# Kernel tuning notes

Hardware: AMD Instinct MI355X
Metric: run time of the kernel (lower is better)

## Reference

```python
import jax, jax.numpy as jnp
import numpy as np

T, N, ENC_DIM, DEC_DIM, ATTN_DIM = 2048, 64, 1024, 1024, 256


def setup_inputs() -> dict:
    key = jax.random.key(0)
    k1, k2, k3, k4, k5 = jax.random.split(key, 5)
    enc_out = jax.random.normal(k1, (T, N, ENC_DIM), dtype=jnp.float32)
    dec_h = jax.random.normal(k2, (N, DEC_DIM), dtype=jnp.float32)
    # Linear weights stored as [out, in] like torch; scaled like default init
    W_e = jax.random.normal(k3, (ATTN_DIM, ENC_DIM), dtype=jnp.float32) / np.sqrt(ENC_DIM)
    W_d = jax.random.normal(k4, (ATTN_DIM, DEC_DIM), dtype=jnp.float32) / np.sqrt(DEC_DIM)
    v = jax.random.normal(k5, (1, ATTN_DIM), dtype=jnp.float32) / np.sqrt(ATTN_DIM)
    return {"enc_out": enc_out, "dec_h": dec_h, "W_e": W_e, "W_d": W_d, "v": v}


def reference(enc_out, dec_h, W_e, W_d, v):
    # e_proj: [T, N, A]; d_proj: [1, N, A]
    e_proj = jnp.einsum('tne,ae->tna', enc_out, W_e)
    d_proj = jnp.einsum('nd,ad->na', dec_h, W_d)[None, :, :]
    # scores: [T, N] = tanh(e+d) @ v
    scores = jnp.einsum('tna,a->tn', jnp.tanh(e_proj + d_proj), v[0])
    alpha = jax.nn.softmax(scores, axis=0)  # softmax over time dim
    ctx = jnp.einsum('tn,tne->ne', alpha, enc_out)  # [N, E]
    return (ctx, alpha)
```

## Files before the change

kernel.cpp:

```cpp
#include <hip/hip_runtime.h>
#include <math.h>

#define T_DIM 2048
#define N_DIM 64
#define E_DIM 1024
#define A_DIM 256
#define TCHUNK 32
#define NCHUNK (T_DIM / TCHUNK)

typedef __bf16 bf16x8 __attribute__((ext_vector_type(8)));
typedef __bf16 bf16x4 __attribute__((ext_vector_type(4)));
typedef float f32x4 __attribute__((ext_vector_type(4)));

__device__ __forceinline__ float tanh_fast(float x) {
    float xc = fminf(fmaxf(x, -15.f), 15.f);
    float e = __expf(2.f * xc);
    return (e - 1.f) / (e + 1.f);
}

__device__ __forceinline__ void lds_barrier() {
    asm volatile("s_waitcnt lgkmcnt(0)\n\ts_barrier" ::: "memory");
}

__global__ __launch_bounds__(256) void prep_kernel(
    const float* __restrict__ W_e, const float* __restrict__ dec_h,
    const float* __restrict__ W_d, __bf16* __restrict__ Wp,
    float* __restrict__ d_proj) {
    __shared__ float dec[E_DIM];
    const int tid = threadIdx.x;
    if (blockIdx.x < 128) {
        const int uid = blockIdx.x * 256 + tid;
        const int a = uid >> 7;
        const int c = uid & 127;
        const float4* src = (const float4*)(W_e + (size_t)a * E_DIM + c * 8);
        float4 x0 = src[0], x1 = src[1];
        bf16x8 o;
        o[0] = (__bf16)x0.x; o[1] = (__bf16)x0.y; o[2] = (__bf16)x0.z; o[3] = (__bf16)x0.w;
        o[4] = (__bf16)x1.x; o[5] = (__bf16)x1.y; o[6] = (__bf16)x1.z; o[7] = (__bf16)x1.w;
        *(bf16x8*)(Wp + ((size_t)c * 256 + a) * 8) = o;
    } else {
        const int n = blockIdx.x - 128;
        reinterpret_cast<float4*>(dec)[tid] =
            reinterpret_cast<const float4*>(dec_h + (size_t)n * E_DIM)[tid];
        __syncthreads();
        const float* w = W_d + (size_t)tid * E_DIM;
        float acc = 0.f;
#pragma unroll 4
        for (int e = 0; e < E_DIM; e += 4) {
            float4 wv = *reinterpret_cast<const float4*>(w + e);
            acc = fmaf(wv.x, dec[e], acc);
            acc = fmaf(wv.y, dec[e + 1], acc);
            acc = fmaf(wv.z, dec[e + 2], acc);
            acc = fmaf(wv.w, dec[e + 3], acc);
        }
        d_proj[n * A_DIM + tid] = acc;
    }
}

__global__ __launch_bounds__(512, 4) void flash_kernel(
    const float* __restrict__ enc, const __bf16* __restrict__ Wp,
    const float* __restrict__ dproj, const float* __restrict__ v,
    float* __restrict__ scores, float* __restrict__ partial,
    float* __restrict__ ms, float* __restrict__ zs) {
    __shared__ __align__(16) __bf16 Atile[TCHUNK * E_DIM];
    float* red = ((float*)Atile) + 16384 - 288;
    float* wls = red + 256;

    const int tid = threadIdx.x;
    const int bid = blockIdx.x;
    const int n = bid & (N_DIM - 1);
    const int c = bid >> 6;
    const int t0 = c * TCHUNK;
    const int wn = tid >> 6;
    const int lane = tid & 63;
    const int lr = lane & 15, lg = lane >> 4;

    f32x4 acc[2][2];
#pragma unroll
    for (int i = 0; i < 2; ++i)
#pragma unroll
        for (int j = 0; j < 2; ++j) acc[i][j] = (f32x4){0.f, 0.f, 0.f, 0.f};

    float vv[2], dp[2];
#pragma unroll
    for (int fn = 0; fn < 2; ++fn) {
        const int a = wn * 32 + fn * 16 + lr;
        vv[fn] = v[a];
        dp[fn] = dproj[n * A_DIM + a];
    }

    const int srow = tid >> 4, sg = tid & 15;
    const int sgg = (sg & 7) >> 1, sbh = sg & 1;
    const int sks = sg >> 3;
    const float* encRow =
        enc + ((size_t)(t0 + srow) * N_DIM + n) * E_DIM + sg * 4;
    const bf16x8* WpV = (const bf16x8*)Wp;

    float4 pa = *(const float4*)encRow;
    float4 pb = *(const float4*)(encRow + 64);
    float4 qa = *(const float4*)(encRow + 128);
    float4 qb = *(const float4*)(encRow + 192);

#pragma unroll
    for (int it = 0; it < 8; ++it) {
        bf16x8 bfr[4][2];
#pragma unroll
        for (int s = 0; s < 4; ++s)
#pragma unroll
            for (int fn = 0; fn < 2; ++fn)
                bfr[s][fn] = WpV[(size_t)(it * 4 + s) * 1024 + lg * 256 +
                                 wn * 32 + fn * 16 + lr];
        {
            const int ks1 = it * 4 + sks, ks2 = ks1 + 2;
            bf16x4 w0, w1;
            w0[0] = (__bf16)pa.x; w0[1] = (__bf16)pa.y;
            w0[2] = (__bf16)pa.z; w0[3] = (__bf16)pa.w;
            w1[0] = (__bf16)pb.x; w1[1] = (__bf16)pb.y;
            w1[2] = (__bf16)pb.z; w1[3] = (__bf16)pb.w;
            const int u1 = ks1 * 128 + sgg * 32 + (srow ^ ((ks1 * 4 + sgg) & 7));
            const int u2 = ks2 * 128 + sgg * 32 + (srow ^ ((ks2 * 4 + sgg) & 7));
            *(bf16x4*)((char*)Atile + u1 * 16 + sbh * 8) = w0;
            *(bf16x4*)((char*)Atile + u2 * 16 + sbh * 8) = w1;
        }
        float4 ra, rb;
        if (it < 6) {
            const float* p = encRow + (it + 2) * 128;
            ra = *(const float4*)p;
            rb = *(const float4*)(p + 64);
        }
        lds_barrier();
#pragma unroll
        for (int s = 0; s < 4; ++s) {
            const int ks = it * 4 + s;
#pragma unroll
            for (int fm = 0; fm < 2; ++fm) {
                const int u =
                    ks * 128 + lg * 32 + ((fm * 16 + lr) ^ ((ks * 4 + lg) & 7));
                bf16x8 af = *(const bf16x8*)((const char*)Atile + u * 16);
                acc[fm][0] = __builtin_amdgcn_mfma_f32_16x16x32_bf16(
                    af, bfr[s][0], acc[fm][0], 0, 0, 0);
                acc[fm][1] = __builtin_amdgcn_mfma_f32_16x16x32_bf16(
                    af, bfr[s][1], acc[fm][1], 0, 0, 0);
            }
        }
        pa = qa; pb = qb;
        qa = ra; qb = rb;
    }

    float pr[2][4];
#pragma unroll
    for (int fm = 0; fm < 2; ++fm) {
#pragma unroll
        for (int reg = 0; reg < 4; ++reg) {
            float p = fmaf(vv[0], tanh_fast(acc[fm][0][reg] + dp[0]), 0.f);
            p = fmaf(vv[1], tanh_fast(acc[fm][1][reg] + dp[1]), p);
            p += __shfl_xor(p, 1);
            p += __shfl_xor(p, 2);
            p += __shfl_xor(p, 4);
            p += __shfl_xor(p, 8);
            pr[fm][reg] = p;
        }
    }
    __syncthreads();
    if (lr == 0) {
#pragma unroll
        for (int fm = 0; fm < 2; ++fm)
#pragma unroll
            for (int reg = 0; reg < 4; ++reg)
                red[wn * 32 + fm * 16 + lg * 4 + reg] = pr[fm][reg];
    }
    __syncthreads();
    if (tid < TCHUNK) {
        float s = 0.f;
#pragma unroll
        for (int w = 0; w < 8; ++w) s += red[w * 32 + tid];
        scores[(t0 + tid) * N_DIM + n] = s;
        if (partial) {
            float m = s;
            m = fmaxf(m, __shfl_xor(m, 1));
            m = fmaxf(m, __shfl_xor(m, 2));
            m = fmaxf(m, __shfl_xor(m, 4));
            m = fmaxf(m, __shfl_xor(m, 8));
            m = fmaxf(m, __shfl_xor(m, 16));
            float w = __expf(s - m);
            float Z = w;
            Z += __shfl_xor(Z, 1);
            Z += __shfl_xor(Z, 2);
            Z += __shfl_xor(Z, 4);
            Z += __shfl_xor(Z, 8);
            Z += __shfl_xor(Z, 16);
            wls[tid] = w;
            if (tid == 0) {
                ms[n * NCHUNK + c] = m;
                zs[n * NCHUNK + c] = Z;
            }
        }
    }
    __syncthreads();

    if (!partial) return;
    const int cs = tid >> 1, rh = tid & 1;
    const int ks = cs >> 3, gg = (cs >> 1) & 3, bh = cs & 1;
    const int colbase = ks * 32 + gg * 8 + bh * 4;
    f32x4 a4 = (f32x4){0.f, 0.f, 0.f, 0.f};
    if (cs < 250) {
        const int q = (ks * 4 + gg) & 7;
        const int ubase = ks * 128 + gg * 32;
#pragma unroll 4
        for (int r = rh * 16; r < rh * 16 + 16; ++r) {
            const float w = wls[r];
            bf16x4 ev = *(const bf16x4*)((const char*)Atile +
                                         (ubase + (r ^ q)) * 16 + bh * 8);
            a4[0] = fmaf(w, (float)ev[0], a4[0]);
            a4[1] = fmaf(w, (float)ev[1], a4[1]);
            a4[2] = fmaf(w, (float)ev[2], a4[2]);
            a4[3] = fmaf(w, (float)ev[3], a4[3]);
        }
    } else {
#pragma unroll 4
        for (int r = rh * 16; r < rh * 16 + 16; ++r) {
            const float w = wls[r];
            float4 ev = *(const float4*)(
                enc + ((size_t)(t0 + r) * N_DIM + n) * E_DIM + colbase);
            a4[0] = fmaf(w, ev.x, a4[0]);
            a4[1] = fmaf(w, ev.y, a4[1]);
            a4[2] = fmaf(w, ev.z, a4[2]);
            a4[3] = fmaf(w, ev.w, a4[3]);
        }
    }
#pragma unroll
    for (int k = 0; k < 4; ++k) a4[k] += __shfl_xor(a4[k], 1);
    if (rh == 0)
        *(f32x4*)(partial + ((size_t)c * N_DIM + n) * E_DIM + colbase) = a4;
}

__global__ __launch_bounds__(256) void combine_kernel(
    const float* __restrict__ partial, const float* __restrict__ ms,
    const float* __restrict__ zs, const float* __restrict__ scores,
    float* __restrict__ ctx, float* __restrict__ alpha) {
    __shared__ float scale[NCHUNK];
    __shared__ float MZ[2];
    const int n = blockIdx.x;
    const int tid = threadIdx.x;
    if (tid < NCHUNK) {
        float m = ms[n * NCHUNK + tid];
        float M = m;
        M = fmaxf(M, __shfl_xor(M, 1));
        M = fmaxf(M, __shfl_xor(M, 2));
        M = fmaxf(M, __shfl_xor(M, 4));
        M = fmaxf(M, __shfl_xor(M, 8));
        M = fmaxf(M, __shfl_xor(M, 16));
        M = fmaxf(M, __shfl_xor(M, 32));
        float e = __expf(m - M);
        float z = zs[n * NCHUNK + tid] * e;
        float Z = z;
        Z += __shfl_xor(Z, 1);
        Z += __shfl_xor(Z, 2);
        Z += __shfl_xor(Z, 4);
        Z += __shfl_xor(Z, 8);
        Z += __shfl_xor(Z, 16);
        Z += __shfl_xor(Z, 32);
        scale[tid] = e;
        if (tid == 0) {
            MZ[0] = M;
            MZ[1] = Z;
        }
    }
    __syncthreads();
    const float M = MZ[0];
    const float invZ = 1.f / MZ[1];
    f32x4 a4 = (f32x4){0.f, 0.f, 0.f, 0.f};
#pragma unroll 4
    for (int c = 0; c < NCHUNK; ++c) {
        const float s = scale[c] * invZ;
        float4 p = *(const float4*)(partial +
                                    ((size_t)c * N_DIM + n) * E_DIM + tid * 4);
        a4[0] = fmaf(s, p.x, a4[0]);
        a4[1] = fmaf(s, p.y, a4[1]);
        a4[2] = fmaf(s, p.z, a4[2]);
        a4[3] = fmaf(s, p.w, a4[3]);
    }
    *(f32x4*)(ctx + (size_t)n * E_DIM + tid * 4) = a4;
    for (int t = tid; t < T_DIM; t += 256)
        alpha[t * N_DIM + n] = __expf(scores[t * N_DIM + n] - M) * invZ;
}

__global__ __launch_bounds__(256) void softmax_kernel(
    const float* __restrict__ scores, float* __restrict__ alpha) {
    __shared__ float red[256];
    const int n = blockIdx.x;
    const int tid = threadIdx.x;
    float m = -3.4e38f;
    for (int t = tid; t < T_DIM; t += 256)
        m = fmaxf(m, scores[t * N_DIM + n]);
    red[tid] = m;
    __syncthreads();
    for (int s = 128; s; s >>= 1) {
        if (tid < s) red[tid] = fmaxf(red[tid], red[tid + s]);
        __syncthreads();
    }
    m = red[0];
    __syncthreads();
    float sum = 0.f;
    for (int t = tid; t < T_DIM; t += 256)
        sum += expf(scores[t * N_DIM + n] - m);
    red[tid] = sum;
    __syncthreads();
    for (int s = 128; s; s >>= 1) {
        if (tid < s) red[tid] += red[tid + s];
        __syncthreads();
    }
    const float inv = 1.f / red[0];
    for (int t = tid; t < T_DIM; t += 256)
        alpha[t * N_DIM + n] = expf(scores[t * N_DIM + n] - m) * inv;
}

__global__ __launch_bounds__(256) void ctx_f32(const float* __restrict__ enc,
                                               const float* __restrict__ alpha,
                                               float* __restrict__ ctx) {
    const int n = blockIdx.x;
    const int tid = threadIdx.x;
    float4 acc = {0.f, 0.f, 0.f, 0.f};
    for (int t = 0; t < T_DIM; ++t) {
        const float al = alpha[t * N_DIM + n];
        float4 ev = *reinterpret_cast<const float4*>(
            enc + (size_t)(t * N_DIM + n) * E_DIM + tid * 4);
        acc.x = fmaf(al, ev.x, acc.x);
        acc.y = fmaf(al, ev.y, acc.y);
        acc.z = fmaf(al, ev.z, acc.z);
        acc.w = fmaf(al, ev.w, acc.w);
    }
    *reinterpret_cast<float4*>(ctx + (size_t)n * E_DIM + tid * 4) = acc;
}

extern "C" void kernel_launch(void* const* d_in, const int* in_sizes, int n_in,
                              void* d_out, int out_size, void* d_ws,
                              size_t ws_size, hipStream_t stream) {
    const float* enc = (const float*)d_in[0];
    const float* dec_h = (const float*)d_in[1];
    const float* W_e = (const float*)d_in[2];
    const float* W_d = (const float*)d_in[3];
    const float* v = (const float*)d_in[4];

    float* out = (float*)d_out;
    float* ctx = out;
    float* alpha = out + 65536;

    float* ws = (float*)d_ws;
    float* d_proj = ws;
    float* scores = ws + 16384;
    __bf16* Wp = (__bf16*)(ws + 147456);
    float* ms = ws + 278528;
    float* zs = ws + 282624;
    float* partial = ws + 286720;

    const size_t need =
        (size_t)(286720 + NCHUNK * N_DIM * E_DIM) * sizeof(float);
    const bool big = ws_size >= need;

    prep_kernel<<<192, 256, 0, stream>>>(W_e, dec_h, W_d, Wp, d_proj);
    flash_kernel<<<T_DIM / TCHUNK * N_DIM, 512, 0, stream>>>(
        enc, Wp, d_proj, v, scores, big ? partial : nullptr, ms, zs);
    if (big) {
        combine_kernel<<<N_DIM, 256, 0, stream>>>(partial, ms, zs, scores,
                                                  ctx, alpha);
    } else {
        softmax_kernel<<<N_DIM, 256, 0, stream>>>(scores, alpha);
        ctx_f32<<<N_DIM, 256, 0, stream>>>(enc, alpha, ctx);
    }
}
```

Baseline: 228.4 us.

## Restructure score GEMM staging with wider enc loads, B-fragment prefetch, nontemporal access

Each thread now loads 16 contiguous floats of the encoder row per stage instead of two float4 pairs, and the K loop is cut to 4 outer iterations of 8 k-steps with full bf16x8 LDS stores. W fragments are double-buffered in registers so the next pair of k-steps is prefetched while the current MFMAs run. Encoder loads and partial-context stores use nontemporal hints to avoid polluting cache. This adds register pressure and changes the LDS write pattern, which may affect occupancy or bank conflicts. Note that the context pass re-reads enc_out, so the nontemporal hint could hurt reuse.

```diff
diff --git a/kernel.cpp b/kernel.cpp
--- a/kernel.cpp
+++ b/kernel.cpp
@@ -20,6 +20,13 @@
 
 __device__ __forceinline__ void lds_barrier() {
     asm volatile("s_waitcnt lgkmcnt(0)\n\ts_barrier" ::: "memory");
+}
+
+__device__ __forceinline__ f32x4 ldnt(const float* p) {
+    return __builtin_nontemporal_load((const f32x4*)p);
+}
+__device__ __forceinline__ void stnt(float* p, f32x4 v) {
+    __builtin_nontemporal_store(v, (f32x4*)p);
 }
 
 __global__ __launch_bounds__(256) void prep_kernel(
@@ -90,61 +97,74 @@
     }
 
     const int srow = tid >> 4, sg = tid & 15;
-    const int sgg = (sg & 7) >> 1, sbh = sg & 1;
-    const int sks = sg >> 3;
     const float* encRow =
-        enc + ((size_t)(t0 + srow) * N_DIM + n) * E_DIM + sg * 4;
+        enc + ((size_t)(t0 + srow) * N_DIM + n) * E_DIM + sg * 16;
     const bf16x8* WpV = (const bf16x8*)Wp;
-
-    float4 pa = *(const float4*)encRow;
-    float4 pb = *(const float4*)(encRow + 64);
-    float4 qa = *(const float4*)(encRow + 128);
-    float4 qb = *(const float4*)(encRow + 192);
-
-#pragma unroll
-    for (int it = 0; it < 8; ++it) {
-        bf16x8 bfr[4][2];
-#pragma unroll
-        for (int s = 0; s < 4; ++s)
-#pragma unroll
-            for (int fn = 0; fn < 2; ++fn)
-                bfr[s][fn] = WpV[(size_t)(it * 4 + s) * 1024 + lg * 256 +
-                                 wn * 32 + fn * 16 + lr];
+    const int bfoff = lg * 256 + wn * 32 + lr;
+    const int sks_base = sg >> 1;
+    const int sg0 = (sg & 1) * 2;
+
+    f32x4 a0 = ldnt(encRow), a1 = ldnt(encRow + 4), a2 = ldnt(encRow + 8),
+          a3 = ldnt(encRow + 12);
+    bf16x8 Bcur[2][2];
+#pragma unroll
+    for (int s = 0; s < 2; ++s)
+#pragma unroll
+        for (int fn = 0; fn < 2; ++fn)
+            Bcur[s][fn] = WpV[(size_t)s * 1024 + bfoff + fn * 16];
+
+#pragma unroll
+    for (int it = 0; it < 4; ++it) {
         {
-            const int ks1 = it * 4 + sks, ks2 = ks1 + 2;
-            bf16x4 w0, w1;
-            w0[0] = (__bf16)pa.x; w0[1] = (__bf16)pa.y;
-            w0[2] = (__bf16)pa.z; w0[3] = (__bf16)pa.w;
-            w1[0] = (__bf16)pb.x; w1[1] = (__bf16)pb.y;
-            w1[2] = (__bf16)pb.z; w1[3] = (__bf16)pb.w;
-            const int u1 = ks1 * 128 + sgg * 32 + (srow ^ ((ks1 * 4 + sgg) & 7));
-            const int u2 = ks2 * 128 + sgg * 32 + (srow ^ ((ks2 * 4 + sgg) & 7));
-            *(bf16x4*)((char*)Atile + u1 * 16 + sbh * 8) = w0;
-            *(bf16x4*)((char*)Atile + u2 * 16 + sbh * 8) = w1;
-        }
-        float4 ra, rb;
-        if (it < 6) {
-            const float* p = encRow + (it + 2) * 128;
-            ra = *(const float4*)p;
-            rb = *(const float4*)(p + 64);
+            const int ks = it * 8 + sks_base;
+            bf16x8 p0, p1;
+            p0[0] = (__bf16)a0[0]; p0[1] = (__bf16)a0[1]; p0[2] = (__bf16)a0[2]; p0[3] = (__bf16)a0[3];
+            p0[4] = (__bf16)a1[0]; p0[5] = (__bf16)a1[1]; p0[6] = (__bf16)a1[2]; p0[7] = (__bf16)a1[3];
+            p1[0] = (__bf16)a2[0]; p1[1] = (__bf16)a2[1]; p1[2] = (__bf16)a2[2]; p1[3] = (__bf16)a2[3];
+            p1[4] = (__bf16)a3[0]; p1[5] = (__bf16)a3[1]; p1[6] = (__bf16)a3[2]; p1[7] = (__bf16)a3[3];
+            const int u0 = ks * 128 + sg0 * 32 + (srow ^ ((ks * 4 + sg0) & 7));
+            const int u1 =
+                ks * 128 + (sg0 + 1) * 32 + (srow ^ ((ks * 4 + sg0 + 1) & 7));
+            *(bf16x8*)((char*)Atile + u0 * 16) = p0;
+            *(bf16x8*)((char*)Atile + u1 * 16) = p1;
+        }
+        if (it < 3) {
+            const float* p = encRow + (it + 1) * 256;
+            a0 = ldnt(p); a1 = ldnt(p + 4); a2 = ldnt(p + 8); a3 = ldnt(p + 12);
         }
         lds_barrier();
 #pragma unroll
-        for (int s = 0; s < 4; ++s) {
-            const int ks = it * 4 + s;
-#pragma unroll
-            for (int fm = 0; fm < 2; ++fm) {
-                const int u =
-                    ks * 128 + lg * 32 + ((fm * 16 + lr) ^ ((ks * 4 + lg) & 7));
-                bf16x8 af = *(const bf16x8*)((const char*)Atile + u * 16);
-                acc[fm][0] = __builtin_amdgcn_mfma_f32_16x16x32_bf16(
-                    af, bfr[s][0], acc[fm][0], 0, 0, 0);
-                acc[fm][1] = __builtin_amdgcn_mfma_f32_16x16x32_bf16(
-                    af, bfr[s][1], acc[fm][1], 0, 0, 0);
+        for (int b = 0; b < 4; ++b) {
+            const int ksb = it * 8 + b * 2;
+            bf16x8 Bnxt[2][2];
+            if (!(it == 3 && b == 3)) {
+                const int ksn = (b < 3) ? ksb + 2 : (it + 1) * 8;
+#pragma unroll
+                for (int s = 0; s < 2; ++s)
+#pragma unroll
+                    for (int fn = 0; fn < 2; ++fn)
+                        Bnxt[s][fn] =
+                            WpV[(size_t)(ksn + s) * 1024 + bfoff + fn * 16];
             }
-        }
-        pa = qa; pb = qb;
-        qa = ra; qb = rb;
+#pragma unroll
+            for (int s = 0; s < 2; ++s) {
+                const int ks = ksb + s;
+#pragma unroll
+                for (int fm = 0; fm < 2; ++fm) {
+                    const int u = ks * 128 + lg * 32 +
+                                  ((fm * 16 + lr) ^ ((ks * 4 + lg) & 7));
+                    bf16x8 af = *(const bf16x8*)((const char*)Atile + u * 16);
+                    acc[fm][0] = __builtin_amdgcn_mfma_f32_16x16x32_bf16(
+                        af, Bcur[s][0], acc[fm][0], 0, 0, 0);
+                    acc[fm][1] = __builtin_amdgcn_mfma_f32_16x16x32_bf16(
+                        af, Bcur[s][1], acc[fm][1], 0, 0, 0);
+                }
+            }
+#pragma unroll
+            for (int s = 0; s < 2; ++s)
+#pragma unroll
+                for (int fn = 0; fn < 2; ++fn) Bcur[s][fn] = Bnxt[s][fn];
+        }
     }
 
     float pr[2][4];
@@ -231,7 +251,7 @@
 #pragma unroll
     for (int k = 0; k < 4; ++k) a4[k] += __shfl_xor(a4[k], 1);
     if (rh == 0)
-        *(f32x4*)(partial + ((size_t)c * N_DIM + n) * E_DIM + colbase) = a4;
+        stnt(partial + ((size_t)c * N_DIM + n) * E_DIM + colbase, a4);
 }
 
 __global__ __launch_bounds__(256) void combine_kernel(
```

Result: slower. 278.4 us (+21.9%).
